# Optimization experiments

Measured on AMD Instinct MI355X. Metric: run time of the kernel, lower is better.

Reference implementation:

```python
import jax, jax.numpy as jnp
import numpy as np

C = 64
CK = C // 8  # query/key channels

def setup_inputs() -> dict:
    key = jax.random.key(0)
    ks = jax.random.split(key, 8)
    x = jax.random.normal(ks[0], (4, C, 16, 16, 16), dtype=jnp.float32)
    # 1x1x1 Conv3d weights collapse to [out_ch, in_ch] matrices
    wq = jax.random.normal(ks[1], (CK, C), dtype=jnp.float32) * (1.0 / np.sqrt(C))
    bq = jax.random.normal(ks[2], (CK,), dtype=jnp.float32) * 0.01
    wk = jax.random.normal(ks[3], (CK, C), dtype=jnp.float32) * (1.0 / np.sqrt(C))
    bk = jax.random.normal(ks[4], (CK,), dtype=jnp.float32) * 0.01
    wv = jax.random.normal(ks[5], (C, C), dtype=jnp.float32) * (1.0 / np.sqrt(C))
    bv = jax.random.normal(ks[6], (C,), dtype=jnp.float32) * 0.01
    gamma = jnp.ones((1,), dtype=jnp.float32) * 0.5  # nonzero so attention path affects output
    return {"x": x, "wq": wq, "bq": bq, "wk": wk, "bk": bk, "wv": wv, "bv": bv, "gamma": gamma}

def reference(x, wq, bq, wk, bk, wv, bv, gamma):
    B, Cc, D, H, W = x.shape
    N = D * H * W
    xf = x.reshape(B, Cc, N)  # [B, C, N]
    q = jnp.einsum('kc,bcn->bkn', wq, xf) + bq[None, :, None]  # [B, CK, N]
    k = jnp.einsum('kc,bcn->bkn', wk, xf) + bk[None, :, None]  # [B, CK, N]
    v = jnp.einsum('oc,bcn->bon', wv, xf) + bv[None, :, None]  # [B, C, N]
    # energy[b,i,j] = sum_k q[b,k,i] * k[b,k,j]; softmax over j (no scaling, per source)
    energy = jnp.einsum('bki,bkj->bij', q, k)  # [B, N, N]
    attn = jax.nn.softmax(energy, axis=-1)
    # out[b,c,i] = sum_j v[b,c,j] * attn[b,i,j]
    out = jnp.einsum('bcj,bij->bci', v, attn)  # [B, C, N]
    out = out.reshape(B, Cc, D, H, W)
    return gamma * out + x
```

## Files before the change

### kernel.cpp

```cpp
#include <hip/hip_runtime.h>
#include <hip/hip_bf16.h>

#define BATCH  4
#define CDIM   64
#define CKD    8
#define NPOS   4096
#define RLN2   1.44269504f
#define SH2    25.96851039f
#define ECL2   14.42695041f
#define PTP    72

typedef _Float16 f16x8 __attribute__((ext_vector_type(8)));
typedef float    f32x4 __attribute__((ext_vector_type(4)));

__device__ __forceinline__ f16x8 pack8(const float* e) {
    f16x8 v;
#pragma unroll
    for (int i = 0; i < 8; ++i) v[i] = (_Float16)e[i];
    return v;
}

__global__ __launch_bounds__(256) void proj_kernel(
    const float* __restrict__ x,
    const float* __restrict__ wq, const float* __restrict__ bq,
    const float* __restrict__ wk, const float* __restrict__ bk,
    const float* __restrict__ wv, const float* __restrict__ bv,
    _Float16* __restrict__ qh, _Float16* __restrict__ kh,
    _Float16* __restrict__ vswz)
{
    const int g    = blockIdx.x * 256 + threadIdx.x;
    const int part = g >> 14;
    const int pos  = g & 16383;
    const int b    = pos >> 12;
    const int n    = pos & 4095;
    const int c0   = part * 16;

    const float* xb = x + (size_t)b * CDIM * NPOS + n;

    float vacc[16];
#pragma unroll
    for (int o = 0; o < 16; ++o) vacc[o] = 0.f;

    if (part < 2) {
        const float* wqk = (part == 0) ? wq : wk;
        const float* bqk = (part == 0) ? bq : bk;
        const float scl  = (part == 0) ? RLN2 : 1.0f;
        float qacc[8];
#pragma unroll
        for (int o = 0; o < 8; ++o) qacc[o] = 0.f;
#pragma unroll 4
        for (int c = 0; c < CDIM; ++c) {
            const float xv = xb[(size_t)c * NPOS];
#pragma unroll
            for (int o = 0; o < 8; ++o)  qacc[o] = fmaf(wqk[o * CDIM + c], xv, qacc[o]);
#pragma unroll
            for (int o = 0; o < 16; ++o) vacc[o] = fmaf(wv[(c0 + o) * CDIM + c], xv, vacc[o]);
        }
        f16x8 qv;
#pragma unroll
        for (int o = 0; o < 8; ++o) qv[o] = (_Float16)((qacc[o] + bqk[o]) * scl);
        _Float16* dst = ((part == 0) ? qh : kh) + ((size_t)(b * NPOS + n)) * CKD;
        *(f16x8*)dst = qv;
    } else {
#pragma unroll 4
        for (int c = 0; c < CDIM; ++c) {
            const float xv = xb[(size_t)c * NPOS];
#pragma unroll
            for (int o = 0; o < 16; ++o) vacc[o] = fmaf(wv[(c0 + o) * CDIM + c], xv, vacc[o]);
        }
    }
    const int jq = (n >> 2) & 3;
    const int ju = ((n >> 4) & 1) * 4 + (n & 3);
    const size_t vbase = (size_t)(b * 128 + (n >> 5)) * 2048 + jq * 8 + ju;
#pragma unroll
    for (int o = 0; o < 16; ++o)
        vswz[vbase + (size_t)(c0 + o) * 32] = (_Float16)(vacc[o] + bv[c0 + o]);
}

template<int NSPLIT>
__global__ __launch_bounds__(256, 4) void attn_kernel(
    const _Float16* __restrict__ qh, const _Float16* __restrict__ kh,
    const _Float16* __restrict__ vswz,
    __hip_bfloat16* __restrict__ po, float* __restrict__ pl)
{
    constexpr int JCHUNK = NPOS / NSPLIT;
    constexpr int NIT32  = JCHUNK / 32;

    __shared__ __hip_bfloat16 pt[4][16][PTP];

    const int bid   = blockIdx.x;
    const int split = bid & (NSPLIT - 1);
    const int itile = (bid / NSPLIT) & 31;
    const int b     = bid / (NSPLIT * 32);
    const int tid   = threadIdx.x;
    const int wave  = tid >> 6;
    const int lane  = tid & 63;
    const int quad  = lane >> 4;
    const int m16   = lane & 15;

    const int i0 = itile * 128 + wave * 32;

    f16x8 qa0 = *(const f16x8*)(qh + ((size_t)(b * NPOS + i0 + m16)) * CKD);
    f16x8 qa1 = *(const f16x8*)(qh + ((size_t)(b * NPOS + i0 + 16 + m16)) * CKD);
    if (quad != 0) { qa0 = (f16x8){}; qa1 = (f16x8){}; }

    const _Float16* kp = kh + ((size_t)(b * NPOS + split * JCHUNK) + (size_t)m16) * CKD;
    const _Float16* vp = vswz + (size_t)b * 262144
                       + (size_t)split * (JCHUNK / 32) * 2048
                       + (size_t)(m16 * 32 + quad * 8);

    f32x4 acc0[4], acc1[4];
#pragma unroll
    for (int nb = 0; nb < 4; ++nb) {
        acc0[nb] = (f32x4){0.f, 0.f, 0.f, 0.f};
        acc1[nb] = (f32x4){0.f, 0.f, 0.f, 0.f};
    }
    float ls0 = 0.f, ls1 = 0.f;
    const f32x4 csh = {-SH2, -SH2, -SH2, -SH2};

    f16x8 kfa = *(const f16x8*)kp;
    f16x8 kfb = *(const f16x8*)(kp + 16 * CKD);
    f16x8 vf0 = *(const f16x8*)(vp);
    f16x8 vf1 = *(const f16x8*)(vp + 512);
    f16x8 vf2 = *(const f16x8*)(vp + 1024);
    f16x8 vf3 = *(const f16x8*)(vp + 1536);

#pragma unroll 2
    for (int it = 0; it < NIT32; ++it) {
        kp += 32 * CKD;
        vp += 2048;
        const f16x8 kfa_n = *(const f16x8*)kp;
        const f16x8 kfb_n = *(const f16x8*)(kp + 16 * CKD);
        const f16x8 vf0_n = *(const f16x8*)(vp);
        const f16x8 vf1_n = *(const f16x8*)(vp + 512);
        const f16x8 vf2_n = *(const f16x8*)(vp + 1024);
        const f16x8 vf3_n = *(const f16x8*)(vp + 1536);

        const f32x4 s0a = __builtin_amdgcn_mfma_f32_16x16x32_f16(kfa, qa0, csh, 0, 0, 0);
        const f32x4 s0b = __builtin_amdgcn_mfma_f32_16x16x32_f16(kfb, qa0, csh, 0, 0, 0);
        const f32x4 s1a = __builtin_amdgcn_mfma_f32_16x16x32_f16(kfa, qa1, csh, 0, 0, 0);
        const f32x4 s1b = __builtin_amdgcn_mfma_f32_16x16x32_f16(kfb, qa1, csh, 0, 0, 0);

        float e0[8], e1[8];
#pragma unroll
        for (int r = 0; r < 4; ++r) {
            e0[r]     = __builtin_exp2f(fminf(s0a[r], ECL2));
            e0[4 + r] = __builtin_exp2f(fminf(s0b[r], ECL2));
            e1[r]     = __builtin_exp2f(fminf(s1a[r], ECL2));
            e1[4 + r] = __builtin_exp2f(fminf(s1b[r], ECL2));
        }
        ls0 += ((e0[0] + e0[1]) + (e0[2] + e0[3])) + ((e0[4] + e0[5]) + (e0[6] + e0[7]));
        ls1 += ((e1[0] + e1[1]) + (e1[2] + e1[3])) + ((e1[4] + e1[5]) + (e1[6] + e1[7]));

        const f16x8 pa0 = pack8(e0);
        const f16x8 pa1 = pack8(e1);

        acc0[0] = __builtin_amdgcn_mfma_f32_16x16x32_f16(pa0, vf0, acc0[0], 0, 0, 0);
        acc1[0] = __builtin_amdgcn_mfma_f32_16x16x32_f16(pa1, vf0, acc1[0], 0, 0, 0);
        acc0[1] = __builtin_amdgcn_mfma_f32_16x16x32_f16(pa0, vf1, acc0[1], 0, 0, 0);
        acc1[1] = __builtin_amdgcn_mfma_f32_16x16x32_f16(pa1, vf1, acc1[1], 0, 0, 0);
        acc0[2] = __builtin_amdgcn_mfma_f32_16x16x32_f16(pa0, vf2, acc0[2], 0, 0, 0);
        acc1[2] = __builtin_amdgcn_mfma_f32_16x16x32_f16(pa1, vf2, acc1[2], 0, 0, 0);
        acc0[3] = __builtin_amdgcn_mfma_f32_16x16x32_f16(pa0, vf3, acc0[3], 0, 0, 0);
        acc1[3] = __builtin_amdgcn_mfma_f32_16x16x32_f16(pa1, vf3, acc1[3], 0, 0, 0);

        kfa = kfa_n; kfb = kfb_n;
        vf0 = vf0_n; vf1 = vf1_n; vf2 = vf2_n; vf3 = vf3_n;
    }

    ls0 += __shfl_xor(ls0, 16);
    ls0 += __shfl_xor(ls0, 32);
    ls1 += __shfl_xor(ls1, 16);
    ls1 += __shfl_xor(ls1, 32);

    const int sbx = split * BATCH + b;
    if (quad == 0) {
        pl[(size_t)sbx * NPOS + i0 + m16]      = ls0;
        pl[(size_t)sbx * NPOS + i0 + 16 + m16] = ls1;
    }

    __hip_bfloat16* ept = &pt[wave][0][0];

#define EPILOG(ACC, IOFS)                                                     \
    do {                                                                      \
        _Pragma("unroll")                                                     \
        for (int nb = 0; nb < 4; ++nb)                                        \
            _Pragma("unroll")                                                 \
            for (int r = 0; r < 4; ++r)                                       \
                ept[(quad * 4 + r) * PTP + nb * 16 + m16] =                   \
                    __float2bfloat16(ACC[nb][r]);                             \
        _Pragma("unroll")                                                     \
        for (int g2 = 0; g2 < 16; ++g2) {                                     \
            const int c = quad + g2 * 4;                                      \
            po[((size_t)sbx * CDIM + c) * NPOS + i0 + (IOFS) + m16] =         \
                ept[m16 * PTP + c];                                           \
        }                                                                     \
    } while (0)

    EPILOG(acc0, 0);
    EPILOG(acc1, 16);
#undef EPILOG
}

template<int NSPLIT>
__global__ __launch_bounds__(256) void combine_kernel(
    const float* __restrict__ x,
    const __hip_bfloat16* __restrict__ po, const float* __restrict__ pl,
    const float* __restrict__ gamma, float* __restrict__ out)
{
    const int t  = blockIdx.x * 256 + threadIdx.x;
    const int i4 = (t & 1023) * 4;
    const int c  = (t >> 10) & 63;
    const int b  = t >> 16;

    const unsigned short* pou = (const unsigned short*)po;

    float L0 = 0.f, L1 = 0.f, L2 = 0.f, L3 = 0.f;
    float O0 = 0.f, O1 = 0.f, O2 = 0.f, O3 = 0.f;
#pragma unroll
    for (int s = 0; s < NSPLIT; ++s) {
        const size_t sb = (size_t)(s * BATCH + b);
        const float4 lv = *(const float4*)(pl + sb * NPOS + i4);
        const ushort4 pv = *(const ushort4*)(pou + (sb * CDIM + c) * NPOS + i4);
        L0 += lv.x; L1 += lv.y; L2 += lv.z; L3 += lv.w;
        O0 += __uint_as_float((unsigned)pv.x << 16);
        O1 += __uint_as_float((unsigned)pv.y << 16);
        O2 += __uint_as_float((unsigned)pv.z << 16);
        O3 += __uint_as_float((unsigned)pv.w << 16);
    }
    const float g = gamma[0];
    const size_t xi = ((size_t)(b * CDIM + c)) * NPOS + i4;
    const float4 xv = *(const float4*)(x + xi);
    float4 o;
    o.x = fmaf(g, O0 / L0, xv.x);
    o.y = fmaf(g, O1 / L1, xv.y);
    o.z = fmaf(g, O2 / L2, xv.z);
    o.w = fmaf(g, O3 / L3, xv.w);
    *(float4*)(out + xi) = o;
}

extern "C" void kernel_launch(void* const* d_in, const int* in_sizes, int n_in,
                              void* d_out, int out_size, void* d_ws, size_t ws_size,
                              hipStream_t stream)
{
    const float* x     = (const float*)d_in[0];
    const float* wq    = (const float*)d_in[1];
    const float* bq    = (const float*)d_in[2];
    const float* wk    = (const float*)d_in[3];
    const float* bk    = (const float*)d_in[4];
    const float* wv    = (const float*)d_in[5];
    const float* bv    = (const float*)d_in[6];
    const float* gamma = (const float*)d_in[7];
    float* out = (float*)d_out;

    char* ws = (char*)d_ws;
    _Float16*       qh   = (_Float16*)(ws);
    _Float16*       kh   = (_Float16*)(ws + (256 << 10));
    _Float16*       vswz = (_Float16*)(ws + (512 << 10));
    __hip_bfloat16* po   = (__hip_bfloat16*)(ws + (2560 << 10));

    const size_t po8_end = (2560ull << 10) + 8ull * 4 * CDIM * NPOS * 2;
    const size_t need8   = po8_end + 8ull * 4 * NPOS * 4;

    proj_kernel<<<256, 256, 0, stream>>>(x, wq, bq, wk, bk, wv, bv, qh, kh, vswz);

    if (ws_size >= need8) {
        float* pl = (float*)(ws + po8_end);
        attn_kernel<8><<<BATCH * 32 * 8, 256, 0, stream>>>(qh, kh, vswz, po, pl);
        combine_kernel<8><<<1024, 256, 0, stream>>>(x, po, pl, gamma, out);
    } else {
        const size_t po4_end = (2560ull << 10) + 4ull * 4 * CDIM * NPOS * 2;
        float* pl = (float*)(ws + po4_end);
        attn_kernel<4><<<BATCH * 32 * 4, 256, 0, stream>>>(qh, kh, vswz, po, pl);
        combine_kernel<4><<<1024, 256, 0, stream>>>(x, po, pl, gamma, out);
    }
}
```

Baseline: 133.0 us.

## Restructure projection kernel with shared-memory x tile; drop manual prefetch in attention

The projection kernel now launches 1024 blocks, each staging a 64x16 tile of x into shared memory. Every thread computes 5 of the 80 output channels (q, k and v) for one position using float4 weight loads, replacing the old scheme where each thread re-read x for 16 or 24 outputs. This raises parallelism and cuts redundant reads of x, but it adds a sync and turns q/k stores into scalar half writes. Separately, the attention loop's explicit register double-buffering of K/V is removed and the loads are issued inline, leaving scheduling to the compiler and possibly exposing load latency.

Result: slower. 255.2 us (+91.9%).

```diff
diff --git a/kernel.cpp b/kernel.cpp
--- a/kernel.cpp
+++ b/kernel.cpp
@@ -20,7 +20,7 @@
     return v;
 }
 
-__global__ __launch_bounds__(256) void proj_kernel(
+__global__ __launch_bounds__(256, 4) void proj_kernel(
     const float* __restrict__ x,
     const float* __restrict__ wq, const float* __restrict__ bq,
     const float* __restrict__ wk, const float* __restrict__ bk,
@@ -28,53 +28,72 @@
     _Float16* __restrict__ qh, _Float16* __restrict__ kh,
     _Float16* __restrict__ vswz)
 {
-    const int g    = blockIdx.x * 256 + threadIdx.x;
-    const int part = g >> 14;
-    const int pos  = g & 16383;
-    const int b    = pos >> 12;
-    const int n    = pos & 4095;
-    const int c0   = part * 16;
-
-    const float* xb = x + (size_t)b * CDIM * NPOS + n;
-
-    float vacc[16];
-#pragma unroll
-    for (int o = 0; o < 16; ++o) vacc[o] = 0.f;
-
-    if (part < 2) {
-        const float* wqk = (part == 0) ? wq : wk;
-        const float* bqk = (part == 0) ? bq : bk;
-        const float scl  = (part == 0) ? RLN2 : 1.0f;
-        float qacc[8];
-#pragma unroll
-        for (int o = 0; o < 8; ++o) qacc[o] = 0.f;
-#pragma unroll 4
-        for (int c = 0; c < CDIM; ++c) {
-            const float xv = xb[(size_t)c * NPOS];
-#pragma unroll
-            for (int o = 0; o < 8; ++o)  qacc[o] = fmaf(wqk[o * CDIM + c], xv, qacc[o]);
-#pragma unroll
-            for (int o = 0; o < 16; ++o) vacc[o] = fmaf(wv[(c0 + o) * CDIM + c], xv, vacc[o]);
-        }
-        f16x8 qv;
-#pragma unroll
-        for (int o = 0; o < 8; ++o) qv[o] = (_Float16)((qacc[o] + bqk[o]) * scl);
-        _Float16* dst = ((part == 0) ? qh : kh) + ((size_t)(b * NPOS + n)) * CKD;
-        *(f16x8*)dst = qv;
-    } else {
-#pragma unroll 4
-        for (int c = 0; c < CDIM; ++c) {
-            const float xv = xb[(size_t)c * NPOS];
-#pragma unroll
-            for (int o = 0; o < 16; ++o) vacc[o] = fmaf(wv[(c0 + o) * CDIM + c], xv, vacc[o]);
-        }
-    }
+    __shared__ float xs[64 * 16];
+
+    const int bid = blockIdx.x;
+    const int b   = bid >> 8;
+    const int n0  = (bid & 255) * 16;
+    const int t   = threadIdx.x;
+
+    {
+        const int c  = t >> 2;
+        const int q4 = (t & 3) * 4;
+        const float4 xv = *(const float4*)(x + (size_t)b * CDIM * NPOS + (size_t)c * NPOS + n0 + q4);
+        xs[c * 16 + q4 + 0] = xv.x;
+        xs[c * 16 + q4 + 1] = xv.y;
+        xs[c * 16 + q4 + 2] = xv.z;
+        xs[c * 16 + q4 + 3] = xv.w;
+    }
+    __syncthreads();
+
+    const int nl = t >> 4;
+    const int og = t & 15;
+    const int n  = n0 + nl;
+
+    const float* rp[5];
+#pragma unroll
+    for (int j = 0; j < 5; ++j) {
+        const int o = og * 5 + j;
+        rp[j] = (o < 8) ? (wq + o * CDIM)
+              : (o < 16) ? (wk + (o - 8) * CDIM)
+                         : (wv + (o - 16) * CDIM);
+    }
+
+    float acc[5] = {0.f, 0.f, 0.f, 0.f, 0.f};
+#pragma unroll
+    for (int cc = 0; cc < 16; ++cc) {
+        float4 w[5];
+#pragma unroll
+        for (int j = 0; j < 5; ++j) w[j] = *(const float4*)(rp[j] + cc * 4);
+        const float x0 = xs[(cc * 4 + 0) * 16 + nl];
+        const float x1 = xs[(cc * 4 + 1) * 16 + nl];
+        const float x2 = xs[(cc * 4 + 2) * 16 + nl];
+        const float x3 = xs[(cc * 4 + 3) * 16 + nl];
+#pragma unroll
+        for (int j = 0; j < 5; ++j) {
+            acc[j] = fmaf(w[j].x, x0, acc[j]);
+            acc[j] = fmaf(w[j].y, x1, acc[j]);
+            acc[j] = fmaf(w[j].z, x2, acc[j]);
+            acc[j] = fmaf(w[j].w, x3, acc[j]);
+        }
+    }
+
     const int jq = (n >> 2) & 3;
     const int ju = ((n >> 4) & 1) * 4 + (n & 3);
     const size_t vbase = (size_t)(b * 128 + (n >> 5)) * 2048 + jq * 8 + ju;
-#pragma unroll
-    for (int o = 0; o < 16; ++o)
-        vswz[vbase + (size_t)(c0 + o) * 32] = (_Float16)(vacc[o] + bv[c0 + o]);
+
+#pragma unroll
+    for (int j = 0; j < 5; ++j) {
+        const int o = og * 5 + j;
+        if (o < 8) {
+            qh[((size_t)(b * NPOS + n)) * CKD + o] = (_Float16)((acc[j] + bq[o]) * RLN2);
+        } else if (o < 16) {
+            kh[((size_t)(b * NPOS + n)) * CKD + (o - 8)] = (_Float16)(acc[j] + bk[o - 8]);
+        } else {
+            const int ch = o - 16;
+            vswz[vbase + (size_t)ch * 32] = (_Float16)(acc[j] + bv[ch]);
+        }
+    }
 }
 
 template<int NSPLIT>
@@ -118,23 +137,10 @@
     float ls0 = 0.f, ls1 = 0.f;
     const f32x4 csh = {-SH2, -SH2, -SH2, -SH2};
 
-    f16x8 kfa = *(const f16x8*)kp;
-    f16x8 kfb = *(const f16x8*)(kp + 16 * CKD);
-    f16x8 vf0 = *(const f16x8*)(vp);
-    f16x8 vf1 = *(const f16x8*)(vp + 512);
-    f16x8 vf2 = *(const f16x8*)(vp + 1024);
-    f16x8 vf3 = *(const f16x8*)(vp + 1536);
-
 #pragma unroll 2
     for (int it = 0; it < NIT32; ++it) {
-        kp += 32 * CKD;
-        vp += 2048;
-        const f16x8 kfa_n = *(const f16x8*)kp;
-        const f16x8 kfb_n = *(const f16x8*)(kp + 16 * CKD);
-        const f16x8 vf0_n = *(const f16x8*)(vp);
-        const f16x8 vf1_n = *(const f16x8*)(vp + 512);
-        const f16x8 vf2_n = *(const f16x8*)(vp + 1024);
-        const f16x8 vf3_n = *(const f16x8*)(vp + 1536);
+        const f16x8 kfa = *(const f16x8*)kp;
+        const f16x8 kfb = *(const f16x8*)(kp + 16 * CKD);
 
         const f32x4 s0a = __builtin_amdgcn_mfma_f32_16x16x32_f16(kfa, qa0, csh, 0, 0, 0);
         const f32x4 s0b = __builtin_amdgcn_mfma_f32_16x16x32_f16(kfb, qa0, csh, 0, 0, 0);
@@ -155,17 +161,14 @@
         const f16x8 pa0 = pack8(e0);
         const f16x8 pa1 = pack8(e1);
 
-        acc0[0] = __builtin_amdgcn_mfma_f32_16x16x32_f16(pa0, vf0, acc0[0], 0, 0, 0);
-        acc1[0] = __builtin_amdgcn_mfma_f32_16x16x32_f16(pa1, vf0, acc1[0], 0, 0, 0);
-        acc0[1] = __builtin_amdgcn_mfma_f32_16x16x32_f16(pa0, vf1, acc0[1], 0, 0, 0);
-        acc1[1] = __builtin_amdgcn_mfma_f32_16x16x32_f16(pa1, vf1, acc1[1], 0, 0, 0);
-        acc0[2] = __builtin_amdgcn_mfma_f32_16x16x32_f16(pa0, vf2, acc0[2], 0, 0, 0);
-        acc1[2] = __builtin_amdgcn_mfma_f32_16x16x32_f16(pa1, vf2, acc1[2], 0, 0, 0);
-        acc0[3] = __builtin_amdgcn_mfma_f32_16x16x32_f16(pa0, vf3, acc0[3], 0, 0, 0);
-        acc1[3] = __builtin_amdgcn_mfma_f32_16x16x32_f16(pa1, vf3, acc1[3], 0, 0, 0);
-
-        kfa = kfa_n; kfb = kfb_n;
-        vf0 = vf0_n; vf1 = vf1_n; vf2 = vf2_n; vf3 = vf3_n;
+#pragma unroll
+        for (int nb = 0; nb < 4; ++nb) {
+            const f16x8 vb = *(const f16x8*)(vp + (size_t)nb * 512);
+            acc0[nb] = __builtin_amdgcn_mfma_f32_16x16x32_f16(pa0, vb, acc0[nb], 0, 0, 0);
+            acc1[nb] = __builtin_amdgcn_mfma_f32_16x16x32_f16(pa1, vb, acc1[nb], 0, 0, 0);
+        }
+        kp += 32 * CKD;
+        vp += 2048;
     }
 
     ls0 += __shfl_xor(ls0, 16);
@@ -262,7 +265,7 @@
     const size_t po8_end = (2560ull << 10) + 8ull * 4 * CDIM * NPOS * 2;
     const size_t need8   = po8_end + 8ull * 4 * NPOS * 4;
 
-    proj_kernel<<<256, 256, 0, stream>>>(x, wq, bq, wk, bk, wv, bv, qh, kh, vswz);
+    proj_kernel<<<1024, 256, 0, stream>>>(x, wq, bq, wk, bk, wv, bv, qh, kh, vswz);
 
     if (ws_size >= need8) {
         float* pl = (float*)(ws + po8_end);
```

## Split projection channel reduction across four waves and drop manual prefetch in attention

Applied to the files above, without the earlier changes.

The projection kernel now assigns 64 positions per block and splits the 64-channel reduction across four waves. Partial sums are reduced through shared memory, and the grid grows from 256 to 1024 blocks to raise occupancy and memory parallelism. The attention loop drops its explicit software prefetch of the K and V fragments and loads them in-iteration, which lowers register pressure but leaves latency hiding to the compiler and occupancy. The combine launch count is unchanged, only rewritten as an expression.

New measurement: 124.1 us. -6.7%, faster.

```diff
diff --git a/kernel.cpp b/kernel.cpp
--- a/kernel.cpp
+++ b/kernel.cpp
@@ -20,7 +20,7 @@
     return v;
 }
 
-__global__ __launch_bounds__(256) void proj_kernel(
+__global__ __launch_bounds__(256, 4) void proj_kernel(
     const float* __restrict__ x,
     const float* __restrict__ wq, const float* __restrict__ bq,
     const float* __restrict__ wk, const float* __restrict__ bk,
@@ -28,47 +28,81 @@
     _Float16* __restrict__ qh, _Float16* __restrict__ kh,
     _Float16* __restrict__ vswz)
 {
-    const int g    = blockIdx.x * 256 + threadIdx.x;
-    const int part = g >> 14;
-    const int pos  = g & 16383;
+    __shared__ float red[64 * 73];
+
+    const int bid  = blockIdx.x;
+    const int part = bid >> 8;
+    const int tid  = threadIdx.x;
+    const int s    = tid & 63;
+    const int h    = tid >> 6;
+    const int pos  = (bid & 255) * 64 + s;
     const int b    = pos >> 12;
     const int n    = pos & 4095;
     const int c0   = part * 16;
+    const int cl0  = h * 16;
 
     const float* xb = x + (size_t)b * CDIM * NPOS + n;
 
     float vacc[16];
 #pragma unroll
     for (int o = 0; o < 16; ++o) vacc[o] = 0.f;
+    float qacc[8] = {0.f, 0.f, 0.f, 0.f, 0.f, 0.f, 0.f, 0.f};
 
     if (part < 2) {
         const float* wqk = (part == 0) ? wq : wk;
+#pragma unroll
+        for (int cc = 0; cc < 16; ++cc) {
+            const int c = cl0 + cc;
+            const float xv = xb[(size_t)c * NPOS];
+#pragma unroll
+            for (int o = 0; o < 8; ++o)  qacc[o] = fmaf(wqk[o * CDIM + c], xv, qacc[o]);
+#pragma unroll
+            for (int o = 0; o < 16; ++o) vacc[o] = fmaf(wv[(c0 + o) * CDIM + c], xv, vacc[o]);
+        }
+    } else {
+#pragma unroll
+        for (int cc = 0; cc < 16; ++cc) {
+            const int c = cl0 + cc;
+            const float xv = xb[(size_t)c * NPOS];
+#pragma unroll
+            for (int o = 0; o < 16; ++o) vacc[o] = fmaf(wv[(c0 + o) * CDIM + c], xv, vacc[o]);
+        }
+    }
+
+    float* rs = red + s * 73;
+    if (h != 0) {
+        float* rh = rs + (h - 1) * 24;
+        if (part < 2) {
+#pragma unroll
+            for (int i = 0; i < 8; ++i)  rh[i] = qacc[i];
+#pragma unroll
+            for (int o = 0; o < 16; ++o) rh[8 + o] = vacc[o];
+        } else {
+#pragma unroll
+            for (int o = 0; o < 16; ++o) rh[o] = vacc[o];
+        }
+    }
+    __syncthreads();
+    if (h != 0) return;
+
+    if (part < 2) {
+#pragma unroll
+        for (int i = 0; i < 8; ++i)  qacc[i] += rs[i] + rs[24 + i] + rs[48 + i];
+#pragma unroll
+        for (int o = 0; o < 16; ++o) vacc[o] += rs[8 + o] + rs[32 + o] + rs[56 + o];
+
         const float* bqk = (part == 0) ? bq : bk;
         const float scl  = (part == 0) ? RLN2 : 1.0f;
-        float qacc[8];
-#pragma unroll
-        for (int o = 0; o < 8; ++o) qacc[o] = 0.f;
-#pragma unroll 4
-        for (int c = 0; c < CDIM; ++c) {
-            const float xv = xb[(size_t)c * NPOS];
-#pragma unroll
-            for (int o = 0; o < 8; ++o)  qacc[o] = fmaf(wqk[o * CDIM + c], xv, qacc[o]);
-#pragma unroll
-            for (int o = 0; o < 16; ++o) vacc[o] = fmaf(wv[(c0 + o) * CDIM + c], xv, vacc[o]);
-        }
         f16x8 qv;
 #pragma unroll
         for (int o = 0; o < 8; ++o) qv[o] = (_Float16)((qacc[o] + bqk[o]) * scl);
         _Float16* dst = ((part == 0) ? qh : kh) + ((size_t)(b * NPOS + n)) * CKD;
         *(f16x8*)dst = qv;
     } else {
-#pragma unroll 4
-        for (int c = 0; c < CDIM; ++c) {
-            const float xv = xb[(size_t)c * NPOS];
-#pragma unroll
-            for (int o = 0; o < 16; ++o) vacc[o] = fmaf(wv[(c0 + o) * CDIM + c], xv, vacc[o]);
-        }
-    }
+#pragma unroll
+        for (int o = 0; o < 16; ++o) vacc[o] += rs[o] + rs[24 + o] + rs[48 + o];
+    }
+
     const int jq = (n >> 2) & 3;
     const int ju = ((n >> 4) & 1) * 4 + (n & 3);
     const size_t vbase = (size_t)(b * 128 + (n >> 5)) * 2048 + jq * 8 + ju;
@@ -118,23 +152,10 @@
     float ls0 = 0.f, ls1 = 0.f;
     const f32x4 csh = {-SH2, -SH2, -SH2, -SH2};
 
-    f16x8 kfa = *(const f16x8*)kp;
-    f16x8 kfb = *(const f16x8*)(kp + 16 * CKD);
-    f16x8 vf0 = *(const f16x8*)(vp);
-    f16x8 vf1 = *(const f16x8*)(vp + 512);
-    f16x8 vf2 = *(const f16x8*)(vp + 1024);
-    f16x8 vf3 = *(const f16x8*)(vp + 1536);
-
 #pragma unroll 2
     for (int it = 0; it < NIT32; ++it) {
-        kp += 32 * CKD;
-        vp += 2048;
-        const f16x8 kfa_n = *(const f16x8*)kp;
-        const f16x8 kfb_n = *(const f16x8*)(kp + 16 * CKD);
-        const f16x8 vf0_n = *(const f16x8*)(vp);
-        const f16x8 vf1_n = *(const f16x8*)(vp + 512);
-        const f16x8 vf2_n = *(const f16x8*)(vp + 1024);
-        const f16x8 vf3_n = *(const f16x8*)(vp + 1536);
+        const f16x8 kfa = *(const f16x8*)kp;
+        const f16x8 kfb = *(const f16x8*)(kp + 16 * CKD);
 
         const f32x4 s0a = __builtin_amdgcn_mfma_f32_16x16x32_f16(kfa, qa0, csh, 0, 0, 0);
         const f32x4 s0b = __builtin_amdgcn_mfma_f32_16x16x32_f16(kfb, qa0, csh, 0, 0, 0);
@@ -155,17 +176,14 @@
         const f16x8 pa0 = pack8(e0);
         const f16x8 pa1 = pack8(e1);
 
-        acc0[0] = __builtin_amdgcn_mfma_f32_16x16x32_f16(pa0, vf0, acc0[0], 0, 0, 0);
-        acc1[0] = __builtin_amdgcn_mfma_f32_16x16x32_f16(pa1, vf0, acc1[0], 0, 0, 0);
-        acc0[1] = __builtin_amdgcn_mfma_f32_16x16x32_f16(pa0, vf1, acc0[1], 0, 0, 0);
-        acc1[1] = __builtin_amdgcn_mfma_f32_16x16x32_f16(pa1, vf1, acc1[1], 0, 0, 0);
-        acc0[2] = __builtin_amdgcn_mfma_f32_16x16x32_f16(pa0, vf2, acc0[2], 0, 0, 0);
-        acc1[2] = __builtin_amdgcn_mfma_f32_16x16x32_f16(pa1, vf2, acc1[2], 0, 0, 0);
-        acc0[3] = __builtin_amdgcn_mfma_f32_16x16x32_f16(pa0, vf3, acc0[3], 0, 0, 0);
-        acc1[3] = __builtin_amdgcn_mfma_f32_16x16x32_f16(pa1, vf3, acc1[3], 0, 0, 0);
-
-        kfa = kfa_n; kfb = kfb_n;
-        vf0 = vf0_n; vf1 = vf1_n; vf2 = vf2_n; vf3 = vf3_n;
+#pragma unroll
+        for (int nb = 0; nb < 4; ++nb) {
+            const f16x8 vb = *(const f16x8*)(vp + (size_t)nb * 512);
+            acc0[nb] = __builtin_amdgcn_mfma_f32_16x16x32_f16(pa0, vb, acc0[nb], 0, 0, 0);
+            acc1[nb] = __builtin_amdgcn_mfma_f32_16x16x32_f16(pa1, vb, acc1[nb], 0, 0, 0);
+        }
+        kp += 32 * CKD;
+        vp += 2048;
     }
 
     ls0 += __shfl_xor(ls0, 16);
@@ -262,16 +280,16 @@
     const size_t po8_end = (2560ull << 10) + 8ull * 4 * CDIM * NPOS * 2;
     const size_t need8   = po8_end + 8ull * 4 * NPOS * 4;
 
-    proj_kernel<<<256, 256, 0, stream>>>(x, wq, bq, wk, bk, wv, bv, qh, kh, vswz);
+    proj_kernel<<<1024, 256, 0, stream>>>(x, wq, bq, wk, bk, wv, bv, qh, kh, vswz);
 
     if (ws_size >= need8) {
         float* pl = (float*)(ws + po8_end);
         attn_kernel<8><<<BATCH * 32 * 8, 256, 0, stream>>>(qh, kh, vswz, po, pl);
-        combine_kernel<8><<<1024, 256, 0, stream>>>(x, po, pl, gamma, out);
+        combine_kernel<8><<<4096 / 4, 256, 0, stream>>>(x, po, pl, gamma, out);
     } else {
         const size_t po4_end = (2560ull << 10) + 4ull * 4 * CDIM * NPOS * 2;
         float* pl = (float*)(ws + po4_end);
         attn_kernel<4><<<BATCH * 32 * 4, 256, 0, stream>>>(qh, kh, vswz, po, pl);
-        combine_kernel<4><<<1024, 256, 0, stream>>>(x, po, pl, gamma, out);
-    }
-}
+        combine_kernel<4><<<4096 / 4, 256, 0, stream>>>(x, po, pl, gamma, out);
+    }
+}
```
